# Kernel tuning notes

Measured on AMD Instinct MI355X. Metric: run time of the kernel, lower is better.

## Reference

```python
import jax, jax.numpy as jnp
import numpy as np

B, S, DIN, D, H, NL, DOUT = 1, 1024, 128, 512, 8, 4, 390
HD = D // H
MAXS = 1024  # max_seq_length; Er has 2*MAXS-1 rows
EPS = 1e-5


def _ln(x, g, b):
    m = jnp.mean(x, axis=-1, keepdims=True)
    v = jnp.mean((x - m) ** 2, axis=-1, keepdims=True)
    return (x - m) / jnp.sqrt(v + EPS) * g + b


def setup_inputs() -> dict:
    key = jax.random.key(0)
    ks = jax.random.split(key, 16)
    it = iter(ks)

    def w(shape, scale=0.02):
        return jax.random.normal(next(it), shape, jnp.float32) * scale

    return {
        "x": jax.random.normal(next(it), (B, S, DIN), jnp.float32),
        "emb_W": w((DIN, D)), "emb_b": jnp.zeros((D,), jnp.float32),
        "Wq": w((NL, D, D)), "bq": jnp.zeros((NL, D), jnp.float32),
        "Wk": w((NL, D, D)), "bk": jnp.zeros((NL, D), jnp.float32),
        "Wv": w((NL, D, D)), "bv": jnp.zeros((NL, D), jnp.float32),
        "Wo": w((NL, D, D)), "bo": jnp.zeros((NL, D), jnp.float32),
        "Er": w((NL, 2 * MAXS - 1, HD), 1.0),  # torch.randn init
        "ln1_g": jnp.ones((NL, D), jnp.float32), "ln1_b": jnp.zeros((NL, D), jnp.float32),
        "W1": w((NL, D, 4 * D)), "b1": jnp.zeros((NL, 4 * D), jnp.float32),
        "W2": w((NL, 4 * D, D)), "b2": jnp.zeros((NL, D), jnp.float32),
        "ln2_g": jnp.ones((NL, D), jnp.float32), "ln2_b": jnp.zeros((NL, D), jnp.float32),
        "lnf_g": jnp.ones((D,), jnp.float32), "lnf_b": jnp.zeros((D,), jnp.float32),
        "Wi": w((D, 2 * D)), "bi": jnp.zeros((2 * D,), jnp.float32),
        "Wf": w((2 * D, DOUT)), "bf": jnp.zeros((DOUT,), jnp.float32),
    }


def reference(x, emb_W, emb_b, Wq, bq, Wk, bk, Wv, bv, Wo, bo, Er,
              ln1_g, ln1_b, W1, b1, W2, b2, ln2_g, ln2_b,
              lnf_g, lnf_b, Wi, bi, Wf, bf):
    h = x @ emb_W + emb_b  # (B,S,D)
    # relative index table (S,S): (i - j) + S - 1, shared by all layers
    ri = (jnp.arange(S)[:, None] - jnp.arange(S)[None, :]) + (S - 1)
    scale = 1.0 / jnp.sqrt(jnp.float32(HD))
    for l in range(NL):
        res = h
        n = _ln(h, ln1_g[l], ln1_b[l])
        q = (n @ Wq[l] + bq[l]).reshape(B, S, H, HD).transpose(0, 2, 1, 3)  # (B,H,S,HD)
        k = (n @ Wk[l] + bk[l]).reshape(B, S, H, HD).transpose(0, 2, 1, 3)
        v = (n @ Wv[l] + bv[l]).reshape(B, S, H, HD).transpose(0, 2, 1, 3)
        scores = jnp.einsum('bhsd,bhtd->bhst', q, k) * scale  # (B,H,S,S)
        E = Er[l][ri]  # (S,S,HD) gathered relative embeddings
        rel = jnp.einsum('bhsd,std->bhst', q, E)  # note: NOT scaled (faithful)
        attn = jax.nn.softmax(scores + rel, axis=-1)  # no causal mask in source
        o = jnp.einsum('bhst,bhtd->bhsd', attn, v)
        o = o.transpose(0, 2, 1, 3).reshape(B, S, D)
        h = res + (o @ Wo[l] + bo[l])
        res = h
        n = _ln(h, ln2_g[l], ln2_b[l])
        f = jax.nn.gelu(n @ W1[l] + b1[l], approximate=False) @ W2[l] + b2[l]
        h = res + f
    h = _ln(h, lnf_g, lnf_b)
    h = jax.nn.gelu(h @ Wi + bi, approximate=False)
    return h @ Wf + bf  # (B,S,DOUT)
```

## Files before the change

### kernel.cpp

```cpp
#include <hip/hip_runtime.h>
#include <hip/hip_bf16.h>
#include <math.h>

#define SEQ 1024
#define DM 512
#define NH 8
#define HD 64
#define NLAYER 4
#define DIN 128
#define DFF 2048
#define DOUT 390
#define ERROWS 2047
#define NSPLIT 4

using u16 = unsigned short;
typedef __attribute__((ext_vector_type(8))) short short8;
typedef __attribute__((ext_vector_type(4))) float f32x4;

typedef __attribute__((address_space(1))) const u16 gas_u16;
typedef __attribute__((address_space(3))) u16 las_u16;

__device__ inline void gload_lds16(const u16* g, u16* l){
  __builtin_amdgcn_global_load_lds((gas_u16*)g, (las_u16*)l, 16, 0, 0);
}

__device__ inline u16 f2bf(float f){
  __hip_bfloat16 h = __float2bfloat16(f);
  return *(u16*)&h;
}
__device__ inline float bf2f(u16 u){
  __hip_bfloat16 h; *(u16*)&h = u;
  return __bfloat162float(h);
}

__global__ __launch_bounds__(256)
void prep_k(const float* __restrict__ x, const float* __restrict__ Er,
            const float* __restrict__ bq, const float* __restrict__ bk,
            const float* __restrict__ bv,
            const float* __restrict__ emb_W, const float* __restrict__ Wq,
            const float* __restrict__ Wk, const float* __restrict__ Wv,
            const float* __restrict__ Wo, const float* __restrict__ W1,
            const float* __restrict__ W2, const float* __restrict__ Wi,
            const float* __restrict__ Wf,
            u16* __restrict__ xb, u16* __restrict__ erB,
            float* __restrict__ qkvbias,
            u16* __restrict__ embT, u16* __restrict__ wqkvT,
            u16* __restrict__ woT, u16* __restrict__ w1T,
            u16* __restrict__ w2T, u16* __restrict__ wiT,
            u16* __restrict__ wfT)
{
  __shared__ float Ls[64][65];
  int b = blockIdx.x;
  const int tid = threadIdx.x;

  if (b < 128){
    int i = (b * 256 + tid) * 4;
    float4 v = *(const float4*)(x + i);
    xb[i+0]=f2bf(v.x); xb[i+1]=f2bf(v.y); xb[i+2]=f2bf(v.z); xb[i+3]=f2bf(v.w);
    return;
  }
  b -= 128;
  if (b < 512){
    int i = (b * 256 + tid) * 4;
    if (i < NLAYER * ERROWS * HD){
      float4 v = *(const float4*)(Er + i);
      erB[i+0]=f2bf(v.x); erB[i+1]=f2bf(v.y); erB[i+2]=f2bf(v.z); erB[i+3]=f2bf(v.w);
    }
    return;
  }
  b -= 512;
  if (b < 24){
    int i = b * 256 + tid;
    int l = i / 1536, c = i - l * 1536;
    float v = (c < 512) ? bq[l * 512 + c]
            : (c < 1024) ? bk[l * 512 + c - 512]
                         : bv[l * 512 + c - 1024];
    qkvbias[i] = v;
    return;
  }
  b -= 24;

  const float* W; u16* WT; int K, N, k0, n0;
  if (b < 16){
    W = emb_W; WT = embT; K = DIN; N = DM;
    k0 = (b & 1) * 64; n0 = (b >> 1) * 64;
  } else if (b < 1040){
    int i = b - 16, fam = i >> 8, w2 = i & 255, z = w2 >> 6, t2 = w2 & 63;
    K = DM; N = DM; k0 = (t2 & 7) * 64; n0 = (t2 >> 3) * 64;
    const float* Wsrc = (fam == 0) ? Wq : (fam == 1) ? Wk : (fam == 2) ? Wv : Wo;
    W = Wsrc + (long)z * DM * DM;
    WT = (fam < 3) ? wqkvT + (long)z * 1536 * DM + (long)fam * 512 * DM
                   : woT + (long)z * DM * DM;
  } else if (b < 2064){
    int i = b - 1040, z = i >> 8, w2 = i & 255;
    K = DM; N = DFF; k0 = (w2 & 7) * 64; n0 = (w2 >> 3) * 64;
    W = W1 + (long)z * DM * DFF; WT = w1T + (long)z * DFF * DM;
  } else if (b < 3088){
    int i = b - 2064, z = i >> 8, w2 = i & 255;
    K = DFF; N = DM; k0 = (w2 & 31) * 64; n0 = (w2 >> 5) * 64;
    W = W2 + (long)z * DFF * DM; WT = w2T + (long)z * DM * DFF;
  } else if (b < 3216){
    int i = b - 3088;
    K = DM; N = 2 * DM; k0 = (i & 7) * 64; n0 = (i >> 3) * 64;
    W = Wi; WT = wiT;
  } else {
    int i = b - 3216;
    K = 2 * DM; N = DOUT; k0 = (i & 15) * 64; n0 = (i >> 4) * 64;
    W = Wf; WT = wfT;
  }

  const int cr = (tid & 15) * 4, rr0 = tid >> 4;
#pragma unroll
  for (int rr = 0; rr < 4; rr++){
    int row = rr0 + rr * 16;
    const float* wp = W + (size_t)(k0 + row) * N + n0 + cr;
#pragma unroll
    for (int j = 0; j < 4; j++)
      Ls[row][cr + j] = (n0 + cr + j < N) ? wp[j] : 0.f;
  }
  __syncthreads();
  const int nrow = tid >> 2, kc = (tid & 3) * 16;
  const bool valid = (n0 + nrow) < N;
  u16 buf[16];
#pragma unroll
  for (int j = 0; j < 16; j++)
    buf[j] = valid ? f2bf(Ls[kc + j][nrow]) : (u16)0;
  u16* out = WT + (size_t)(n0 + nrow) * K + k0 + kc;
  ((uint4*)out)[0] = ((uint4*)buf)[0];
  ((uint4*)out)[1] = ((uint4*)buf)[1];
}

template<bool GELU, bool RES, bool BIAS, bool OUTBF>
__global__ __launch_bounds__(256)
void mgemm(const u16* __restrict__ A, const u16* __restrict__ B,
           const float* __restrict__ bias, const float* __restrict__ res,
           void* __restrict__ Cout, int N, int K,
           int lda, int ldb, int ldc)
{
  __shared__ u16 As[32][64];
  __shared__ u16 Bs[64][64];
  const int tid = threadIdx.x;
  const int row0 = blockIdx.y * 32, n0 = blockIdx.x * 64;
  const int w = tid >> 6, lane = tid & 63, m = lane & 15, quad = lane >> 4;
  const int rowg = w >> 1, colp = w & 1;

  const int arr  = w * 8 + (lane >> 3);
  const int acg  = ((lane & 7) ^ (arr & 7)) * 8;
  const int brr0 = w * 16 + (lane >> 3);
  const int brr1 = brr0 + 8;
  const int bcg0 = ((lane & 7) ^ (brr0 & 7)) * 8;
  const int bcg1 = ((lane & 7) ^ (brr1 & 7)) * 8;

  const int sw  = m & 7;
  const int cS0 = ((quad ^ sw) << 3);
  const int cS1 = (((quad + 4) ^ sw) << 3);

  f32x4 acc[2];
  acc[0] = (f32x4){0.f,0.f,0.f,0.f};
  acc[1] = (f32x4){0.f,0.f,0.f,0.f};

  for (int k0 = 0; k0 < K; k0 += 64){
    gload_lds16(A + (long)(row0 + arr)  * lda + k0 + acg,  &As[w * 8][0]);
    gload_lds16(B + (long)(n0 + brr0) * ldb + k0 + bcg0, &Bs[w * 16][0]);
    gload_lds16(B + (long)(n0 + brr1) * ldb + k0 + bcg1, &Bs[w * 16 + 8][0]);
    __syncthreads();
    short8 a0 = *(const short8*)&As[rowg * 16 + m][cS0];
    short8 a1 = *(const short8*)&As[rowg * 16 + m][cS1];
#pragma unroll
    for (int c = 0; c < 2; c++){
      int colg = colp * 2 + c;
      short8 b0 = *(const short8*)&Bs[colg * 16 + m][cS0];
      short8 b1 = *(const short8*)&Bs[colg * 16 + m][cS1];
      acc[c] = __builtin_amdgcn_mfma_f32_16x16x32_bf16(a0, b0, acc[c], 0, 0, 0);
      acc[c] = __builtin_amdgcn_mfma_f32_16x16x32_bf16(a1, b1, acc[c], 0, 0, 0);
    }
    __syncthreads();
  }

#pragma unroll
  for (int c = 0; c < 2; c++){
    int col = n0 + (colp * 2 + c) * 16 + m;
    if (col < N){
#pragma unroll
      for (int r = 0; r < 4; r++){
        int row = row0 + rowg * 16 + quad * 4 + r;
        float val = acc[c][r];
        if (BIAS) val += bias[col];
        if (RES)  val += res[(long)row * ldc + col];
        if (GELU) val = 0.5f * val * (1.f + erff(val * 0.70710678118f));
        if (OUTBF) ((u16*)Cout)[(long)row * ldc + col] = f2bf(val);
        else      ((float*)Cout)[(long)row * ldc + col] = val;
      }
    }
  }
}

__global__ __launch_bounds__(256)
void ln_k(const float* __restrict__ x, const float* __restrict__ g,
          const float* __restrict__ b, u16* __restrict__ out)
{
  const int w = threadIdx.x >> 6, lane = threadIdx.x & 63;
  const int r = blockIdx.x * 4 + w;
  const float4* xr = (const float4*)(x + (long)r * DM + lane * 8);
  float4 v0 = xr[0], v1 = xr[1];
  float s = v0.x+v0.y+v0.z+v0.w + v1.x+v1.y+v1.z+v1.w;
  float q = v0.x*v0.x+v0.y*v0.y+v0.z*v0.z+v0.w*v0.w
          + v1.x*v1.x+v1.y*v1.y+v1.z*v1.z+v1.w*v1.w;
#pragma unroll
  for (int off = 1; off < 64; off <<= 1){
    s += __shfl_xor(s, off);
    q += __shfl_xor(q, off);
  }
  float mn = s * (1.f / DM);
  float inv = rsqrtf(q * (1.f / DM) - mn * mn + 1e-5f);
  const float4* gp = (const float4*)(g + lane * 8);
  const float4* bp = (const float4*)(b + lane * 8);
  float4 g0 = gp[0], g1 = gp[1], b0 = bp[0], b1 = bp[1];
  u16 tmp[8];
  tmp[0] = f2bf((v0.x - mn) * inv * g0.x + b0.x);
  tmp[1] = f2bf((v0.y - mn) * inv * g0.y + b0.y);
  tmp[2] = f2bf((v0.z - mn) * inv * g0.z + b0.z);
  tmp[3] = f2bf((v0.w - mn) * inv * g0.w + b0.w);
  tmp[4] = f2bf((v1.x - mn) * inv * g1.x + b1.x);
  tmp[5] = f2bf((v1.y - mn) * inv * g1.y + b1.y);
  tmp[6] = f2bf((v1.z - mn) * inv * g1.z + b1.z);
  tmp[7] = f2bf((v1.w - mn) * inv * g1.w + b1.w);
  *(uint4*)(out + (long)r * DM + lane * 8) = *(uint4*)tmp;
}

__global__ __launch_bounds__(256)
void flash_k(const u16* __restrict__ qkv, const u16* __restrict__ ErB,
             float* __restrict__ Op, float* __restrict__ ml)
{
  __shared__ u16 Qs[64][72];
  __shared__ u16 Ks[64][72];
  __shared__ u16 VsT[64][72];
  __shared__ u16 Es[128][72];
  __shared__ u16 Ts[64][136];
  __shared__ u16 Ps[64][72];

  const int tid = threadIdx.x;
  const int s0 = blockIdx.x * 64, hh = blockIdx.y, sp = blockIdx.z;
  const int w = tid >> 6, lane = tid & 63, m = lane & 15, quad = lane >> 4;

  {
    const int r = tid >> 2, kc = (tid & 3) * 16;
    const u16* qp = qkv + (size_t)(s0 + r) * 1536 + hh * HD + kc;
    *(uint4*)&Qs[r][kc]     = *(const uint4*)&qp[0];
    *(uint4*)&Qs[r][kc + 8] = *(const uint4*)&qp[8];
  }
  __syncthreads();

  const short8 a0 = *(const short8*)&Qs[w * 16 + m][quad * 8];
  const short8 a1 = *(const short8*)&Qs[w * 16 + m][32 + quad * 8];

  f32x4 accO[4];
#pragma unroll
  for (int c = 0; c < 4; c++) accO[c] = (f32x4){0.f, 0.f, 0.f, 0.f};
  float mrun[4], lrun[4];
#pragma unroll
  for (int r = 0; r < 4; r++){ mrun[r] = -1e30f; lrun[r] = 0.f; }

  const int tbeg = sp * (SEQ / NSPLIT), tend = tbeg + SEQ / NSPLIT;
  for (int t0 = tbeg; t0 < tend; t0 += 64){
    __syncthreads();
    {
      const int r = tid >> 2, kc = (tid & 3) * 16;
      const u16* kp = qkv + (size_t)(t0 + r) * 1536 + 512 + hh * HD + kc;
      *(uint4*)&Ks[r][kc]     = *(const uint4*)&kp[0];
      *(uint4*)&Ks[r][kc + 8] = *(const uint4*)&kp[8];
      const u16* vp = qkv + (size_t)(t0 + r) * 1536 + 1024 + hh * HD + kc;
      uint4 v0 = *(const uint4*)&vp[0];
      uint4 v1 = *(const uint4*)&vp[8];
      const u16* pv0 = (const u16*)&v0;
      const u16* pv1 = (const u16*)&v1;
#pragma unroll
      for (int j = 0; j < 8; j++) VsT[kc + j][r]     = pv0[j];
#pragma unroll
      for (int j = 0; j < 8; j++) VsT[kc + 8 + j][r] = pv1[j];
      const int rb = s0 - t0 + 960;
      for (int idx = tid; idx < 127 * 8; idx += 256){
        int er = idx >> 3, ekc = (idx & 7) * 8;
        *(uint4*)&Es[er][ekc] = *(const uint4*)&ErB[(size_t)(rb + er) * HD + ekc];
      }
      if (tid < 8){ uint4 z = {0,0,0,0}; *(uint4*)&Es[127][tid * 8] = z; }
    }
    __syncthreads();

    f32x4 qk[4], tt[8];
#pragma unroll
    for (int c = 0; c < 4; c++) qk[c] = (f32x4){0.f,0.f,0.f,0.f};
#pragma unroll
    for (int c = 0; c < 8; c++) tt[c] = (f32x4){0.f,0.f,0.f,0.f};
#pragma unroll
    for (int c = 0; c < 4; c++){
      short8 b0 = *(const short8*)&Ks[c * 16 + m][quad * 8];
      short8 b1 = *(const short8*)&Ks[c * 16 + m][32 + quad * 8];
      qk[c] = __builtin_amdgcn_mfma_f32_16x16x32_bf16(a0, b0, qk[c], 0, 0, 0);
      qk[c] = __builtin_amdgcn_mfma_f32_16x16x32_bf16(a1, b1, qk[c], 0, 0, 0);
    }
#pragma unroll
    for (int c = 0; c < 8; c++){
      short8 b0 = *(const short8*)&Es[c * 16 + m][quad * 8];
      short8 b1 = *(const short8*)&Es[c * 16 + m][32 + quad * 8];
      tt[c] = __builtin_amdgcn_mfma_f32_16x16x32_bf16(a0, b0, tt[c], 0, 0, 0);
      tt[c] = __builtin_amdgcn_mfma_f32_16x16x32_bf16(a1, b1, tt[c], 0, 0, 0);
    }
#pragma unroll
    for (int c = 0; c < 8; c++)
#pragma unroll
      for (int r = 0; r < 4; r++)
        Ts[w * 16 + quad * 4 + r][c * 16 + m] = f2bf(tt[c][r]);
    __syncthreads();

    float sv[4][4];
#pragma unroll
    for (int c = 0; c < 4; c++){
      int j = c * 16 + m;
#pragma unroll
      for (int r = 0; r < 4; r++){
        int i = w * 16 + quad * 4 + r;
        sv[c][r] = qk[c][r] * 0.125f + bf2f(Ts[i][i - j + 63]);
      }
    }
    float alpha[4];
#pragma unroll
    for (int r = 0; r < 4; r++){
      float rmax = fmaxf(fmaxf(sv[0][r], sv[1][r]), fmaxf(sv[2][r], sv[3][r]));
#pragma unroll
      for (int off = 1; off < 16; off <<= 1)
        rmax = fmaxf(rmax, __shfl_xor(rmax, off));
      float mnew = fmaxf(mrun[r], rmax);
      alpha[r] = __expf(mrun[r] - mnew);
      mrun[r] = mnew;
      float rsum = 0.f;
#pragma unroll
      for (int c = 0; c < 4; c++){
        float pv = __expf(sv[c][r] - mnew);
        sv[c][r] = pv;
        rsum += pv;
      }
#pragma unroll
      for (int off = 1; off < 16; off <<= 1)
        rsum += __shfl_xor(rsum, off);
      lrun[r] = lrun[r] * alpha[r] + rsum;
    }
#pragma unroll
    for (int c = 0; c < 4; c++)
#pragma unroll
      for (int r = 0; r < 4; r++)
        accO[c][r] *= alpha[r];
#pragma unroll
    for (int c = 0; c < 4; c++)
#pragma unroll
      for (int r = 0; r < 4; r++)
        Ps[w * 16 + quad * 4 + r][c * 16 + m] = f2bf(sv[c][r]);
    __syncthreads();

    short8 pa0 = *(const short8*)&Ps[w * 16 + m][quad * 8];
    short8 pa1 = *(const short8*)&Ps[w * 16 + m][32 + quad * 8];
#pragma unroll
    for (int c = 0; c < 4; c++){
      short8 b0 = *(const short8*)&VsT[c * 16 + m][quad * 8];
      short8 b1 = *(const short8*)&VsT[c * 16 + m][32 + quad * 8];
      accO[c] = __builtin_amdgcn_mfma_f32_16x16x32_bf16(pa0, b0, accO[c], 0, 0, 0);
      accO[c] = __builtin_amdgcn_mfma_f32_16x16x32_bf16(pa1, b1, accO[c], 0, 0, 0);
    }
  }

  const long base = ((long)sp * NH + hh) * SEQ;
#pragma unroll
  for (int c = 0; c < 4; c++){
#pragma unroll
    for (int r = 0; r < 4; r++){
      int row = s0 + w * 16 + quad * 4 + r;
      Op[(base + row) * HD + c * 16 + m] = accO[c][r];
    }
  }
  if (m == 0){
#pragma unroll
    for (int r = 0; r < 4; r++){
      int row = s0 + w * 16 + quad * 4 + r;
      ml[(base + row) * 2 + 0] = mrun[r];
      ml[(base + row) * 2 + 1] = lrun[r];
    }
  }
}

__global__ __launch_bounds__(256)
void fcomb_k(const float* __restrict__ Op, const float* __restrict__ ml,
             u16* __restrict__ o)
{
  const int s = blockIdx.x, tid = threadIdx.x;
  const int hh = tid >> 5, c0 = (tid & 31) * 2;
  float mm[NSPLIT], ll[NSPLIT];
#pragma unroll
  for (int sp = 0; sp < NSPLIT; sp++){
    long b = (((long)sp * NH + hh) * SEQ + s) * 2;
    mm[sp] = ml[b]; ll[sp] = ml[b + 1];
  }
  float ms = fmaxf(fmaxf(mm[0], mm[1]), fmaxf(mm[2], mm[3]));
  float o0 = 0.f, o1 = 0.f, lsum = 0.f;
#pragma unroll
  for (int sp = 0; sp < NSPLIT; sp++){
    float wsp = __expf(mm[sp] - ms);
    lsum += wsp * ll[sp];
    const float* op = Op + (((long)sp * NH + hh) * SEQ + s) * HD + c0;
    o0 += wsp * op[0];
    o1 += wsp * op[1];
  }
  float inv = 1.f / lsum;
  o[(size_t)s * DM + hh * HD + c0]     = f2bf(o0 * inv);
  o[(size_t)s * DM + hh * HD + c0 + 1] = f2bf(o1 * inv);
}

extern "C" void kernel_launch(void* const* d_in, const int* in_sizes, int n_in,
                              void* d_out, int out_size, void* d_ws, size_t ws_size,
                              hipStream_t stream) {
  const float* x     = (const float*)d_in[0];
  const float* emb_W = (const float*)d_in[1];
  const float* emb_b = (const float*)d_in[2];
  const float* Wq    = (const float*)d_in[3];
  const float* bq    = (const float*)d_in[4];
  const float* Wk    = (const float*)d_in[5];
  const float* bk    = (const float*)d_in[6];
  const float* Wv    = (const float*)d_in[7];
  const float* bv    = (const float*)d_in[8];
  const float* Wo    = (const float*)d_in[9];
  const float* bo    = (const float*)d_in[10];
  const float* Er    = (const float*)d_in[11];
  const float* ln1_g = (const float*)d_in[12];
  const float* ln1_b = (const float*)d_in[13];
  const float* W1    = (const float*)d_in[14];
  const float* b1    = (const float*)d_in[15];
  const float* W2    = (const float*)d_in[16];
  const float* b2    = (const float*)d_in[17];
  const float* ln2_g = (const float*)d_in[18];
  const float* ln2_b = (const float*)d_in[19];
  const float* lnf_g = (const float*)d_in[20];
  const float* lnf_b = (const float*)d_in[21];
  const float* Wi    = (const float*)d_in[22];
  const float* bi    = (const float*)d_in[23];
  const float* Wf    = (const float*)d_in[24];
  const float* bfin  = (const float*)d_in[25];

  u16* p = (u16*)d_ws;
  u16* xb    = p; p += SEQ * DIN;
  u16* embT  = p; p += DM * DIN;
  u16* wqkvT = p; p += (size_t)NLAYER * 1536 * DM;
  u16* woT   = p; p += (size_t)NLAYER * DM * DM;
  u16* w1T   = p; p += (size_t)NLAYER * DFF * DM;
  u16* w2T   = p; p += (size_t)NLAYER * DM * DFF;
  u16* wiT   = p; p += (size_t)(2 * DM) * DM;
  u16* wfT   = p; p += (size_t)448 * (2 * DM);
  u16* erB   = p; p += (size_t)NLAYER * ERROWS * HD;
  u16* nb    = p; p += SEQ * DM;
  u16* qkvb  = p; p += (size_t)SEQ * 1536;
  u16* ob    = p; p += SEQ * DM;
  u16* mid   = p; p += (size_t)SEQ * DFF;
  float* qkvbias = (float*)p;
  float* hb  = qkvbias + NLAYER * 1536;
  float* Op  = hb + SEQ * DM;
  float* mlb = Op + (size_t)NSPLIT * NH * SEQ * HD;

  dim3 blk(256);

  prep_k<<<3992, blk, 0, stream>>>(
      x, Er, bq, bk, bv, emb_W, Wq, Wk, Wv, Wo, W1, W2, Wi, Wf,
      xb, erB, qkvbias, embT, wqkvT, woT, w1T, w2T, wiT, wfT);

  dim3 g512(8, 32), gqkv(24, 32), gff(32, 32), gwi(16, 32), gout(7, 32);
  dim3 gfl(16, NH, NSPLIT);
  dim3 gln(SEQ / 4);

  mgemm<false, false, true, false><<<g512, blk, 0, stream>>>(
      xb, embT, emb_b, nullptr, hb, DM, DIN, DIN, DIN, DM);

  for (int l = 0; l < NLAYER; l++) {
    const u16* wqkvT_l = wqkvT + (size_t)l * 1536 * DM;
    const u16* woT_l   = woT + (size_t)l * DM * DM;
    const u16* w1T_l   = w1T + (size_t)l * DFF * DM;
    const u16* w2T_l   = w2T + (size_t)l * DM * DFF;
    const u16* erB_l   = erB + (size_t)l * ERROWS * HD;

    ln_k<<<gln, blk, 0, stream>>>(hb, ln1_g + l * DM, ln1_b + l * DM, nb);
    mgemm<false, false, true, true><<<gqkv, blk, 0, stream>>>(
        nb, wqkvT_l, qkvbias + l * 1536, nullptr, qkvb, 1536, DM, DM, DM, 1536);

    flash_k<<<gfl, blk, 0, stream>>>(qkvb, erB_l, Op, mlb);
    fcomb_k<<<SEQ, blk, 0, stream>>>(Op, mlb, ob);

    mgemm<false, true, true, false><<<g512, blk, 0, stream>>>(
        ob, woT_l, bo + l * DM, hb, hb, DM, DM, DM, DM, DM);

    ln_k<<<gln, blk, 0, stream>>>(hb, ln2_g + l * DM, ln2_b + l * DM, nb);
    mgemm<true, false, true, true><<<gff, blk, 0, stream>>>(
        nb, w1T_l, b1 + l * DFF, nullptr, mid, DFF, DM, DM, DM, DFF);
    mgemm<false, true, true, false><<<g512, blk, 0, stream>>>(
        mid, w2T_l, b2 + l * DM, hb, hb, DM, DFF, DFF, DFF, DM);
  }

  ln_k<<<gln, blk, 0, stream>>>(hb, lnf_g, lnf_b, nb);
  mgemm<true, false, true, true><<<gwi, blk, 0, stream>>>(
      nb, wiT, bi, nullptr, mid, 2 * DM, DM, DM, DM, 2 * DM);
  mgemm<false, false, true, false><<<gout, blk, 0, stream>>>(
      mid, wfT, bfin, nullptr, (float*)d_out, DOUT, 2 * DM, 2 * DM, 2 * DM, DOUT);
}
```

Measured before the change: 458.3 us.

## Replace direct global-to-LDS loads with register prefetch and padded LDS in GEMM

The GEMM kernel stops using global_load_lds with XOR-swizzled LDS tiles. It now loads the next K-tile into registers while the current tile is consumed, and writes to padded LDS rows (stride 72) to avoid bank conflicts. The aim is to overlap global-load latency with MFMA work. Separately, the flash-combine kernel now handles four sequence rows per block and launches a quarter as many blocks. The cost is extra VGPR pressure and an explicit register-to-LDS store step.

```diff
diff --git a/kernel.cpp b/kernel.cpp
--- a/kernel.cpp
+++ b/kernel.cpp
@@ -16,13 +16,6 @@
 using u16 = unsigned short;
 typedef __attribute__((ext_vector_type(8))) short short8;
 typedef __attribute__((ext_vector_type(4))) float f32x4;
-
-typedef __attribute__((address_space(1))) const u16 gas_u16;
-typedef __attribute__((address_space(3))) u16 las_u16;
-
-__device__ inline void gload_lds16(const u16* g, u16* l){
-  __builtin_amdgcn_global_load_lds((gas_u16*)g, (las_u16*)l, 16, 0, 0);
-}
 
 __device__ inline u16 f2bf(float f){
   __hip_bfloat16 h = __float2bfloat16(f);
@@ -137,40 +130,40 @@
            void* __restrict__ Cout, int N, int K,
            int lda, int ldb, int ldc)
 {
-  __shared__ u16 As[32][64];
-  __shared__ u16 Bs[64][64];
+  __shared__ u16 As[32][72];
+  __shared__ u16 Bs[64][72];
   const int tid = threadIdx.x;
   const int row0 = blockIdx.y * 32, n0 = blockIdx.x * 64;
   const int w = tid >> 6, lane = tid & 63, m = lane & 15, quad = lane >> 4;
   const int rowg = w >> 1, colp = w & 1;
-
-  const int arr  = w * 8 + (lane >> 3);
-  const int acg  = ((lane & 7) ^ (arr & 7)) * 8;
-  const int brr0 = w * 16 + (lane >> 3);
-  const int brr1 = brr0 + 8;
-  const int bcg0 = ((lane & 7) ^ (brr0 & 7)) * 8;
-  const int bcg1 = ((lane & 7) ^ (brr1 & 7)) * 8;
-
-  const int sw  = m & 7;
-  const int cS0 = ((quad ^ sw) << 3);
-  const int cS1 = (((quad + 4) ^ sw) << 3);
+  const int ar = tid >> 3, akc = (tid & 7) * 8;
+  const int br = tid >> 2, bkc = (tid & 3) * 16;
 
   f32x4 acc[2];
   acc[0] = (f32x4){0.f,0.f,0.f,0.f};
   acc[1] = (f32x4){0.f,0.f,0.f,0.f};
 
+  uint4 pa  = *(const uint4*)&A[(long)(row0 + ar) * lda + akc];
+  uint4 pb0 = *(const uint4*)&B[(long)(n0 + br) * ldb + bkc];
+  uint4 pb1 = *(const uint4*)&B[(long)(n0 + br) * ldb + bkc + 8];
+
   for (int k0 = 0; k0 < K; k0 += 64){
-    gload_lds16(A + (long)(row0 + arr)  * lda + k0 + acg,  &As[w * 8][0]);
-    gload_lds16(B + (long)(n0 + brr0) * ldb + k0 + bcg0, &Bs[w * 16][0]);
-    gload_lds16(B + (long)(n0 + brr1) * ldb + k0 + bcg1, &Bs[w * 16 + 8][0]);
+    *(uint4*)&As[ar][akc]     = pa;
+    *(uint4*)&Bs[br][bkc]     = pb0;
+    *(uint4*)&Bs[br][bkc + 8] = pb1;
     __syncthreads();
-    short8 a0 = *(const short8*)&As[rowg * 16 + m][cS0];
-    short8 a1 = *(const short8*)&As[rowg * 16 + m][cS1];
+    if (k0 + 64 < K){
+      pa  = *(const uint4*)&A[(long)(row0 + ar) * lda + k0 + 64 + akc];
+      pb0 = *(const uint4*)&B[(long)(n0 + br) * ldb + k0 + 64 + bkc];
+      pb1 = *(const uint4*)&B[(long)(n0 + br) * ldb + k0 + 64 + bkc + 8];
+    }
+    short8 a0 = *(const short8*)&As[rowg * 16 + m][quad * 8];
+    short8 a1 = *(const short8*)&As[rowg * 16 + m][32 + quad * 8];
 #pragma unroll
     for (int c = 0; c < 2; c++){
       int colg = colp * 2 + c;
-      short8 b0 = *(const short8*)&Bs[colg * 16 + m][cS0];
-      short8 b1 = *(const short8*)&Bs[colg * 16 + m][cS1];
+      short8 b0 = *(const short8*)&Bs[colg * 16 + m][quad * 8];
+      short8 b1 = *(const short8*)&Bs[colg * 16 + m][32 + quad * 8];
       acc[c] = __builtin_amdgcn_mfma_f32_16x16x32_bf16(a0, b0, acc[c], 0, 0, 0);
       acc[c] = __builtin_amdgcn_mfma_f32_16x16x32_bf16(a1, b1, acc[c], 0, 0, 0);
     }
@@ -391,27 +384,31 @@
 void fcomb_k(const float* __restrict__ Op, const float* __restrict__ ml,
              u16* __restrict__ o)
 {
-  const int s = blockIdx.x, tid = threadIdx.x;
+  const int tid = threadIdx.x;
   const int hh = tid >> 5, c0 = (tid & 31) * 2;
-  float mm[NSPLIT], ll[NSPLIT];
-#pragma unroll
-  for (int sp = 0; sp < NSPLIT; sp++){
-    long b = (((long)sp * NH + hh) * SEQ + s) * 2;
-    mm[sp] = ml[b]; ll[sp] = ml[b + 1];
-  }
-  float ms = fmaxf(fmaxf(mm[0], mm[1]), fmaxf(mm[2], mm[3]));
-  float o0 = 0.f, o1 = 0.f, lsum = 0.f;
-#pragma unroll
-  for (int sp = 0; sp < NSPLIT; sp++){
-    float wsp = __expf(mm[sp] - ms);
-    lsum += wsp * ll[sp];
-    const float* op = Op + (((long)sp * NH + hh) * SEQ + s) * HD + c0;
-    o0 += wsp * op[0];
-    o1 += wsp * op[1];
-  }
-  float inv = 1.f / lsum;
-  o[(size_t)s * DM + hh * HD + c0]     = f2bf(o0 * inv);
-  o[(size_t)s * DM + hh * HD + c0 + 1] = f2bf(o1 * inv);
+#pragma unroll
+  for (int i = 0; i < 4; i++){
+    const int s = blockIdx.x * 4 + i;
+    float mm[NSPLIT], ll[NSPLIT];
+#pragma unroll
+    for (int sp = 0; sp < NSPLIT; sp++){
+      long b = (((long)sp * NH + hh) * SEQ + s) * 2;
+      mm[sp] = ml[b]; ll[sp] = ml[b + 1];
+    }
+    float ms = fmaxf(fmaxf(mm[0], mm[1]), fmaxf(mm[2], mm[3]));
+    float o0 = 0.f, o1 = 0.f, lsum = 0.f;
+#pragma unroll
+    for (int sp = 0; sp < NSPLIT; sp++){
+      float wsp = __expf(mm[sp] - ms);
+      lsum += wsp * ll[sp];
+      const float* op = Op + (((long)sp * NH + hh) * SEQ + s) * HD + c0;
+      o0 += wsp * op[0];
+      o1 += wsp * op[1];
+    }
+    float inv = 1.f / lsum;
+    o[(size_t)s * DM + hh * HD + c0]     = f2bf(o0 * inv);
+    o[(size_t)s * DM + hh * HD + c0 + 1] = f2bf(o1 * inv);
+  }
 }
 
 extern "C" void kernel_launch(void* const* d_in, const int* in_sizes, int n_in,
@@ -488,7 +485,7 @@
         nb, wqkvT_l, qkvbias + l * 1536, nullptr, qkvb, 1536, DM, DM, DM, 1536);
 
     flash_k<<<gfl, blk, 0, stream>>>(qkvb, erB_l, Op, mlb);
-    fcomb_k<<<SEQ, blk, 0, stream>>>(Op, mlb, ob);
+    fcomb_k<<<SEQ / 4, blk, 0, stream>>>(Op, mlb, ob);
 
     mgemm<false, true, true, false><<<g512, blk, 0, stream>>>(
         ob, woT_l, bo + l * DM, hb, hb, DM, DM, DM, DM, DM);
```

Result: faster. 445.7 us (median of 2 runs) (-2.8%).
